# Kernel tuning notes

Hardware: AMD Instinct MI355X
Metric: run time of the kernel (lower is better)

The kernel has to match this reference:

```python
import jax, jax.numpy as jnp
import numpy as np

NEG_INF = -1e20  # the repo defines INF = 1e20
TOPK = 10


def setup_inputs() -> dict:
    key = jax.random.key(0)
    k1, k2 = jax.random.split(key)
    B, N, D, H = 8, 2048, 512, 512
    context = jax.random.normal(k1, (B, N, D), dtype=jnp.float32)
    ctx_mask = jnp.ones((B, N), dtype=jnp.int32)  # all positions valid
    W = jax.random.normal(k2, (H, D), dtype=jnp.float32) * 0.02  # linear_sim weight
    return {"context": context, "W": W, "ctx_mask": ctx_mask}


def reference(context, W, ctx_mask):
    # context_fc = relu(linear_sim(context))        : [B, N, H]
    ctx_fc = jax.nn.relu(jnp.einsum('bnd,hd->bnh', context, W))
    # attention = context_fc @ context_fc^T         : [B, N, N]
    att = jnp.einsum('bnh,bmh->bnm', ctx_fc, ctx_fc)
    # masked_fill where ctx_mask == 0 (both row and column)
    m = ctx_mask.astype(bool)
    att = jnp.where(m[:, None, :], att, NEG_INF)
    att = jnp.where(m[:, :, None], att, NEG_INF)
    # build_knn_neighbourhood: keep top-k per row, everything else -INF
    k = min(TOPK, att.shape[-1])
    knn_val, knn_ind = jax.lax.top_k(att, k)  # [B, N, k]
    B, N, _ = att.shape
    bi = jnp.arange(B)[:, None, None]
    ri = jnp.arange(N)[None, :, None]
    adj = jnp.full(att.shape, NEG_INF, dtype=att.dtype).at[bi, ri, knn_ind].set(knn_val)
    return adj
```

## Files before the change

kernel.cpp:

```cpp
#include <hip/hip_runtime.h>
#include <hip/hip_bf16.h>

#define NEG_INF -1e20f

typedef __bf16 bf16x8 __attribute__((ext_vector_type(8)));
typedef float  f32x4  __attribute__((ext_vector_type(4)));

__device__ inline unsigned short f2bf(float x) {
    unsigned u = __float_as_uint(x);
    unsigned r = u + 0x7fffu + ((u >> 16) & 1u);
    return (unsigned short)(r >> 16);
}
__device__ inline float bf2f(unsigned short h) {
    return __uint_as_float((unsigned)h << 16);
}
__device__ inline unsigned fkey(float f) {
    unsigned u = __float_as_uint(f);
    return (u & 0x80000000u) ? ~u : (u | 0x80000000u);
}
__device__ inline float unfkey(unsigned k) {
    unsigned fu = (k & 0x80000000u) ? (k ^ 0x80000000u) : ~k;
    return __uint_as_float(fu);
}

__global__ __launch_bounds__(256) void split3_all(
        const float* __restrict__ ctx, const float* __restrict__ W,
        unsigned short* __restrict__ C1, unsigned short* __restrict__ C2,
        unsigned short* __restrict__ C3, unsigned short* __restrict__ W1,
        unsigned short* __restrict__ W2, unsigned short* __restrict__ W3) {
    const int b = blockIdx.x;
    const int t = threadIdx.x;
    const float* src;
    unsigned short *p1, *p2, *p3;
    int base;
    if (b < 2048) { src = ctx; p1 = C1; p2 = C2; p3 = C3; base = b * 1024; }
    else          { src = W;   p1 = W1; p2 = W2; p3 = W3; base = (b - 2048) * 1024; }
#pragma unroll
    for (int it = 0; it < 4; ++it) {
        int i = base + it * 256 + t;
        float4 v = ((const float4*)src)[i];
        ushort4 a, bb, c;
        float r;
        a.x = f2bf(v.x); r = v.x - bf2f(a.x); bb.x = f2bf(r); c.x = f2bf(r - bf2f(bb.x));
        a.y = f2bf(v.y); r = v.y - bf2f(a.y); bb.y = f2bf(r); c.y = f2bf(r - bf2f(bb.y));
        a.z = f2bf(v.z); r = v.z - bf2f(a.z); bb.z = f2bf(r); c.z = f2bf(r - bf2f(bb.z));
        a.w = f2bf(v.w); r = v.w - bf2f(a.w); bb.w = f2bf(r); c.w = f2bf(r - bf2f(bb.w));
        ((ushort4*)p1)[i] = a;
        ((ushort4*)p2)[i] = bb;
        ((ushort4*)p3)[i] = c;
    }
}

__global__ __launch_bounds__(256, 2) void fc_mfma6(
        const unsigned short* __restrict__ A1, const unsigned short* __restrict__ A2,
        const unsigned short* __restrict__ A3, const unsigned short* __restrict__ B1,
        const unsigned short* __restrict__ B2, const unsigned short* __restrict__ B3,
        unsigned short* __restrict__ Fhi, unsigned short* __restrict__ Flo) {
    __shared__ char lds[49152];

    const int t     = threadIdx.x;
    const int mBase = blockIdx.x * 128;
    const int hBase = blockIdx.y * 128;
    const int w = t >> 6, lane = t & 63;
    const int q = lane >> 4, ln = lane & 15;
    const int wn = (w >> 1) * 64;
    const int wm = (w & 1) * 64;

    f32x4 acc[4][4] = {};

    for (int kt = 0; kt < 512; kt += 32) {
#pragma unroll
        for (int p = 0; p < 3; ++p) {
            const unsigned short* pl = (p == 0) ? A1 : (p == 1) ? A2 : A3;
#pragma unroll
            for (int rr = 0; rr < 2; ++rr) {
                int chunk = rr * 256 + t;
                int row   = chunk >> 2;
                int c     = (chunk & 3) ^ ((row >> 1) & 3);
                const unsigned short* g = pl + ((size_t)(mBase + row) * 512 + kt + c * 8);
                char* l = lds + p * 8192 + chunk * 16;
                __builtin_amdgcn_global_load_lds(
                    (const __attribute__((address_space(1))) void*)g,
                    (__attribute__((address_space(3))) void*)l, 16, 0, 0);
            }
        }
#pragma unroll
        for (int p = 0; p < 3; ++p) {
            const unsigned short* pl = (p == 0) ? B1 : (p == 1) ? B2 : B3;
#pragma unroll
            for (int rr = 0; rr < 2; ++rr) {
                int chunk = rr * 256 + t;
                int row   = chunk >> 2;
                int c     = (chunk & 3) ^ ((row >> 1) & 3);
                const unsigned short* g = pl + ((size_t)(hBase + row) * 512 + kt + c * 8);
                char* l = lds + 24576 + p * 8192 + chunk * 16;
                __builtin_amdgcn_global_load_lds(
                    (const __attribute__((address_space(1))) void*)g,
                    (__attribute__((address_space(3))) void*)l, 16, 0, 0);
            }
        }
        __syncthreads();

        bf16x8 a1[4], a2[4], a3[4], b1[4], b2[4], b3[4];
#pragma unroll
        for (int i = 0; i < 4; ++i) {
            int mA = wn + i * 16 + ln;
            int oA = (mA * 4 + (q ^ ((mA >> 1) & 3))) * 16;
            a1[i] = *(const bf16x8*)(lds +     0 + oA);
            a2[i] = *(const bf16x8*)(lds +  8192 + oA);
            a3[i] = *(const bf16x8*)(lds + 16384 + oA);
            int mB = wm + i * 16 + ln;
            int oB = (mB * 4 + (q ^ ((mB >> 1) & 3))) * 16;
            b1[i] = *(const bf16x8*)(lds + 24576 + oB);
            b2[i] = *(const bf16x8*)(lds + 32768 + oB);
            b3[i] = *(const bf16x8*)(lds + 40960 + oB);
        }
#pragma unroll
        for (int i = 0; i < 4; ++i)
#pragma unroll
            for (int j = 0; j < 4; ++j) {
                acc[i][j] = __builtin_amdgcn_mfma_f32_16x16x32_bf16(a1[i], b1[j], acc[i][j], 0, 0, 0);
                acc[i][j] = __builtin_amdgcn_mfma_f32_16x16x32_bf16(a1[i], b2[j], acc[i][j], 0, 0, 0);
                acc[i][j] = __builtin_amdgcn_mfma_f32_16x16x32_bf16(a2[i], b1[j], acc[i][j], 0, 0, 0);
                acc[i][j] = __builtin_amdgcn_mfma_f32_16x16x32_bf16(a2[i], b2[j], acc[i][j], 0, 0, 0);
                acc[i][j] = __builtin_amdgcn_mfma_f32_16x16x32_bf16(a1[i], b3[j], acc[i][j], 0, 0, 0);
                acc[i][j] = __builtin_amdgcn_mfma_f32_16x16x32_bf16(a3[i], b1[j], acc[i][j], 0, 0, 0);
            }
        __syncthreads();
    }

    unsigned* tb = (unsigned*)(lds + w * 4352);
    const int rg = lane >> 4;
    const int c4 = lane & 15;
#pragma unroll
    for (int i = 0; i < 4; ++i) {
#pragma unroll
        for (int j = 0; j < 4; ++j)
#pragma unroll
            for (int r = 0; r < 4; ++r) {
                float v = fmaxf(acc[i][j][r], 0.f);
                unsigned short hi = f2bf(v);
                unsigned short lo = f2bf(v - bf2f(hi));
                tb[(q * 4 + r) * 68 + j * 16 + ln] =
                    (unsigned)hi | ((unsigned)lo << 16);
            }
#pragma unroll
        for (int it = 0; it < 4; ++it) {
            int row = it * 4 + rg;
            uint4 pk = *(const uint4*)&tb[row * 68 + c4 * 4];
            ushort4 h, l;
            h.x = (unsigned short)pk.x; l.x = (unsigned short)(pk.x >> 16);
            h.y = (unsigned short)pk.y; l.y = (unsigned short)(pk.y >> 16);
            h.z = (unsigned short)pk.z; l.z = (unsigned short)(pk.z >> 16);
            h.w = (unsigned short)pk.w; l.w = (unsigned short)(pk.w >> 16);
            size_t off = (size_t)(mBase + wn + i * 16 + row) * 512 + hBase + wm + c4 * 4;
            *(ushort4*)(Fhi + off) = h;
            *(ushort4*)(Flo + off) = l;
        }
    }
}

__global__ __launch_bounds__(256, 3) void att_sym_cand(
        const unsigned short* __restrict__ Fhi, const unsigned short* __restrict__ Flo,
        const int* __restrict__ mask, float* __restrict__ out,
        float* __restrict__ cv2) {
    __shared__ char lds[32768];

    const int t = threadIdx.x;
    const int b = blockIdx.x & 7;
    int p = blockIdx.x >> 3, ti = 0;
    while (p >= 16 - ti) { p -= 16 - ti; ++ti; }
    const int tj = ti + p;
    const int nBase = ti * 128;
    const int mBase = tj * 128;
    const int w    = t >> 6, lane = t & 63;
    const int q    = lane >> 4, ln = lane & 15;
    const int wn   = (w >> 1) * 64;
    const int wm   = (w & 1) * 64;
    const size_t rowB = (size_t)b * 2048;

    f32x4 acc[4][4] = {};

    for (int kt = 0; kt < 512; kt += 32) {
#pragma unroll
        for (int pp = 0; pp < 4; ++pp) {
            const unsigned short* plane = (pp & 1) ? Flo : Fhi;
            int rbase = (pp < 2) ? nBase : mBase;
#pragma unroll
            for (int r = 0; r < 2; ++r) {
                int chunk = r * 256 + t;
                int row   = chunk >> 2;
                int c     = (chunk & 3) ^ ((row >> 1) & 3);
                const unsigned short* g =
                    plane + ((rowB + rbase + row) * 512 + kt + c * 8);
                char* l = lds + pp * 8192 + chunk * 16;
                __builtin_amdgcn_global_load_lds(
                    (const __attribute__((address_space(1))) void*)g,
                    (__attribute__((address_space(3))) void*)l, 16, 0, 0);
            }
        }
        __syncthreads();

        bf16x8 ah[4], al[4], bh[4], bl[4];
#pragma unroll
        for (int i = 0; i < 4; ++i) {
            int mA = wn + i * 16 + ln;
            int oA = (mA * 4 + (q ^ ((mA >> 1) & 3))) * 16;
            ah[i] = *(const bf16x8*)(lds +     0 + oA);
            al[i] = *(const bf16x8*)(lds +  8192 + oA);
            int mB = wm + i * 16 + ln;
            int oB = (mB * 4 + (q ^ ((mB >> 1) & 3))) * 16;
            bh[i] = *(const bf16x8*)(lds + 16384 + oB);
            bl[i] = *(const bf16x8*)(lds + 24576 + oB);
        }
#pragma unroll
        for (int i = 0; i < 4; ++i)
#pragma unroll
            for (int j = 0; j < 4; ++j) {
                acc[i][j] = __builtin_amdgcn_mfma_f32_16x16x32_bf16(ah[i], bh[j], acc[i][j], 0, 0, 0);
                acc[i][j] = __builtin_amdgcn_mfma_f32_16x16x32_bf16(ah[i], bl[j], acc[i][j], 0, 0, 0);
                acc[i][j] = __builtin_amdgcn_mfma_f32_16x16x32_bf16(al[i], bh[j], acc[i][j], 0, 0, 0);
            }
        __syncthreads();
    }

    const int* mb = mask + b * 2048;
    float* outB = out + (size_t)b * 2048 * 2048;
    int cmj[4];
#pragma unroll
    for (int j = 0; j < 4; ++j) cmj[j] = mb[mBase + wm + j * 16 + ln];
    int rmAll[4][4];
#pragma unroll
    for (int i = 0; i < 4; ++i)
#pragma unroll
        for (int r = 0; r < 4; ++r) rmAll[i][r] = mb[nBase + wn + i * 16 + q * 4 + r];

    float* tb = (float*)(lds + w * 4352);
    const int rg = lane >> 4;
    const int c4 = lane & 15;
    const bool mirror = (ti != tj);
#pragma unroll
    for (int i = 0; i < 4; ++i) {
        int n0 = nBase + wn + i * 16;
#pragma unroll
        for (int r = 0; r < 4; ++r) {
            float m4 = NEG_INF;
#pragma unroll
            for (int j = 0; j < 4; ++j) {
                float v = ((rmAll[i][r] != 0) & (cmj[j] != 0)) ? acc[i][j][r] : NEG_INF;
                m4 = fmaxf(m4, v);
            }
            m4 = fmaxf(m4, __shfl_xor(m4, 1, 64));
            m4 = fmaxf(m4, __shfl_xor(m4, 2, 64));
            m4 = fmaxf(m4, __shfl_xor(m4, 4, 64));
            m4 = fmaxf(m4, __shfl_xor(m4, 8, 64));
            if (ln == 0)
                cv2[(rowB + n0 + q * 4 + r) * 32 + tj * 2 + (w & 1)] = m4;
        }
#pragma unroll
        for (int j = 0; j < 4; ++j)
#pragma unroll
            for (int r = 0; r < 4; ++r) {
                float v = ((rmAll[i][r] != 0) & (cmj[j] != 0)) ? acc[i][j][r] : NEG_INF;
                tb[(q * 4 + r) * 68 + j * 16 + ln] = v;
            }
#pragma unroll
        for (int it = 0; it < 4; ++it) {
            int row = it * 4 + rg;
            float4 vv = *(const float4*)&tb[row * 68 + c4 * 4];
            *(float4*)(outB + (size_t)(n0 + row) * 2048 + mBase + wm + c4 * 4) = vv;
        }
        if (mirror) {
#pragma unroll
            for (int ps = 0; ps < 4; ++ps) {
                float4 mv;
                mv.x = tb[(ps * 4 + 0) * 68 + lane];
                mv.y = tb[(ps * 4 + 1) * 68 + lane];
                mv.z = tb[(ps * 4 + 2) * 68 + lane];
                mv.w = tb[(ps * 4 + 3) * 68 + lane];
                *(float4*)(outB + (size_t)(mBase + wm + lane) * 2048 + n0 + ps * 4) = mv;
            }
        }
    }
    if (mirror) {
#pragma unroll
        for (int j = 0; j < 4; ++j) {
            float m16 = NEG_INF;
#pragma unroll
            for (int i2 = 0; i2 < 4; ++i2)
#pragma unroll
                for (int r = 0; r < 4; ++r) {
                    float v = ((rmAll[i2][r] != 0) & (cmj[j] != 0)) ? acc[i2][j][r] : NEG_INF;
                    m16 = fmaxf(m16, v);
                }
            m16 = fmaxf(m16, __shfl_xor(m16, 16, 64));
            m16 = fmaxf(m16, __shfl_xor(m16, 32, 64));
            if (q == 0)
                cv2[(rowB + mBase + wm + j * 16 + ln) * 32 + ti * 2 + (w >> 1)] = m16;
        }
    }
}

__global__ __launch_bounds__(256) void topk_filter(
        const float* __restrict__ cv2, float* __restrict__ att) {
    __shared__ float2 surv[4][64];
    __shared__ float2 win[4][10];

    const int t = threadIdx.x, w = t >> 6, lane = t & 63;
    const size_t R = (size_t)blockIdx.x * 4 + w;
    float* row = att + R * 2048;

    float cnd = (lane < 32) ? cv2[R * 32 + lane] : NEG_INF;
    int rk = 0;
#pragma unroll
    for (int j = 0; j < 32; ++j) {
        float vj = __shfl(cnd, j, 64);
        rk += ((vj > cnd) || (vj == cnd && j < lane)) ? 1 : 0;
    }
    unsigned long long bl = __ballot((lane < 32) && (rk == 9));
    float L = __shfl(cnd, __ffsll(bl) - 1, 64);
    unsigned long long hsel = __ballot((lane < 32) && (cnd >= L));
    const int nsel = (int)__popcll(hsel);

    const bool ok = (nsel <= 16);
    float v[16]; int hcol[16]; bool hv[16];
    if (ok) {
        unsigned long long m = hsel;
#pragma unroll
        for (int k = 0; k < 16; ++k) {
            hv[k] = (m != 0);
            int h = hv[k] ? (__ffsll(m) - 1) : 0;
            m &= (m - 1);
            hcol[k] = h * 64 + lane;
            v[k] = row[h * 64 + lane];
        }
    }

    int nsurv = 0;
    if (ok) {
        const unsigned long long lmask = (1ull << lane) - 1;
#pragma unroll
        for (int k = 0; k < 16; ++k) {
            bool pr = hv[k] && (v[k] >= L);
            unsigned long long pb = __ballot(pr);
            if (pr) {
                int idx = nsurv + (int)__popcll(pb & lmask);
                if (idx < 64) surv[w][idx] = make_float2(v[k], __int_as_float(hcol[k]));
            }
            nsurv += (int)__popcll(pb);
        }
    }

    if (ok && nsurv <= 64) {
        float sv = NEG_INF; int sc = 0x7fffffff;
        if (lane < nsurv) {
            float2 s2 = surv[w][lane];
            sv = s2.x; sc = __float_as_int(s2.y);
        }
        int r2 = 0;
        for (int j = 0; j < nsurv; ++j) {
            float2 sj = surv[w][j];
            int cj = __float_as_int(sj.y);
            r2 += ((sj.x > sv) || (sj.x == sv && cj < sc)) ? 1 : 0;
        }
        if ((lane < nsurv) && (r2 < 10))
            win[w][r2] = make_float2(sv, __int_as_float(sc));
    } else {
        unsigned key[32];
#pragma unroll
        for (int s = 0; s < 8; ++s) {
            float4 vv = *(const float4*)(row + lane * 32 + s * 4);
            key[s * 4 + 0] = fkey(vv.x);
            key[s * 4 + 1] = fkey(vv.y);
            key[s * 4 + 2] = fkey(vv.z);
            key[s * 4 + 3] = fkey(vv.w);
        }
        unsigned h1 = key[0]; int i1 = 0;
#pragma unroll
        for (int j = 1; j < 32; ++j)
            if (key[j] > h1) { h1 = key[j]; i1 = j; }
        unsigned h2 = 0; int i2 = 0;
#pragma unroll
        for (int j = 0; j < 32; ++j) {
            bool okb = (j != i1) && (key[j] > h2);
            h2 = okb ? key[j] : h2;
            i2 = okb ? j : i2;
        }
        bool h2valid = true;
        unsigned taken = 0;
        for (int r = 0; r < 10; ++r) {
            unsigned M = h1;
#pragma unroll
            for (int off = 1; off < 64; off <<= 1) {
                unsigned o = __shfl_xor(M, off, 64);
                M = (o > M) ? o : M;
            }
            unsigned long long ball = __ballot(h1 == M);
            int srcb = __ffsll(ball) - 1;
            int wloc = __shfl(i1, srcb, 64);
            if (lane == r) win[w][r] = make_float2(unfkey(M), __int_as_float(srcb * 32 + wloc));
            if (lane == srcb) {
                taken |= 1u << i1;
                if (h2valid) { h1 = h2; i1 = i2; h2valid = false; }
                else {
                    unsigned bh = 0; int bi = 0;
#pragma unroll
                    for (int j = 0; j < 32; ++j) {
                        bool okb = (((taken >> j) & 1u) == 0u) && (key[j] > bh);
                        bh = okb ? key[j] : bh;
                        bi = okb ? j : bi;
                    }
                    h1 = bh; i1 = bi;
                }
            }
        }
    }

    float wv[10]; int wc[10];
#pragma unroll
    for (int k = 0; k < 10; ++k) {
        float2 wk = win[w][k];
        wv[k] = wk.x; wc[k] = __float_as_int(wk.y);
    }

#pragma unroll
    for (int s = 0; s < 8; ++s) {
        float4 f4 = make_float4(NEG_INF, NEG_INF, NEG_INF, NEG_INF);
        int cb = s * 256 + lane * 4;
#pragma unroll
        for (int k = 0; k < 10; ++k) {
            if ((wc[k] >> 8) == s) {
                f4.x = (wc[k] == cb + 0) ? wv[k] : f4.x;
                f4.y = (wc[k] == cb + 1) ? wv[k] : f4.y;
                f4.z = (wc[k] == cb + 2) ? wv[k] : f4.z;
                f4.w = (wc[k] == cb + 3) ? wv[k] : f4.w;
            }
        }
        ((float4*)row)[s * 64 + lane] = f4;
    }
}

extern "C" void kernel_launch(void* const* d_in, const int* in_sizes, int n_in,
                              void* d_out, int out_size, void* d_ws, size_t ws_size,
                              hipStream_t stream) {
    const float* ctx  = (const float*)d_in[0];
    const float* W    = (const float*)d_in[1];
    const int*   mask = (const int*)d_in[2];
    float* out = (float*)d_out;

    const size_t CN = (size_t)16384 * 512;
    const size_t WN = (size_t)512 * 512;
    unsigned short* C1 = (unsigned short*)d_out;
    unsigned short* C2 = C1 + CN;
    unsigned short* C3 = C2 + CN;
    unsigned short* W1 = C3 + CN;
    unsigned short* W2 = W1 + WN;
    unsigned short* W3 = W2 + WN;

    float* cv2 = (float*)d_ws;
    unsigned short* Fhi = (unsigned short*)(cv2 + (size_t)16384 * 32);
    unsigned short* Flo = Fhi + CN;

    dim3 blk(256);
    split3_all<<<dim3(2112), blk, 0, stream>>>(ctx, W, C1, C2, C3, W1, W2, W3);
    fc_mfma6<<<dim3(128, 4), blk, 0, stream>>>(C1, C2, C3, W1, W2, W3, Fhi, Flo);
    att_sym_cand<<<dim3(1088), blk, 0, stream>>>(Fhi, Flo, mask, out, cv2);
    topk_filter<<<dim3(4096), blk, 0, stream>>>(cv2, out);
}
```

Before: 295.2 us.

## Double-buffer fc GEMM with 512-thread 256x128 tiles and async LDS prefetch

Rewrites the context-projection GEMM kernel to use 512 threads covering a 256x128 output tile. Global-to-LDS loads are double-buffered in dynamic shared memory (about 144KB), and the next K-slice is prefetched while MFMAs run on the current one. The block-wide barriers become explicit vmcnt waits plus s_barrier, and s_setprio is raised around the MFMA section. The aim is to hide load latency and cut synchronisation stalls, at the cost of one block per CU and a large LDS footprint. The epilogue still appears to index LDS per wave, and it is unclear whether the existing epilogue handles the 8 waves and 256-row tile correctly.

```diff
diff --git a/kernel.cpp b/kernel.cpp
--- a/kernel.cpp
+++ b/kernel.cpp
@@ -51,70 +51,79 @@
     }
 }
 
-__global__ __launch_bounds__(256, 2) void fc_mfma6(
+__global__ __launch_bounds__(512, 1) void fc_8ph(
         const unsigned short* __restrict__ A1, const unsigned short* __restrict__ A2,
         const unsigned short* __restrict__ A3, const unsigned short* __restrict__ B1,
         const unsigned short* __restrict__ B2, const unsigned short* __restrict__ B3,
         unsigned short* __restrict__ Fhi, unsigned short* __restrict__ Flo) {
-    __shared__ char lds[49152];
+    extern __shared__ char lds[];
 
     const int t     = threadIdx.x;
-    const int mBase = blockIdx.x * 128;
+    const int mBase = blockIdx.x * 256;
     const int hBase = blockIdx.y * 128;
     const int w = t >> 6, lane = t & 63;
     const int q = lane >> 4, ln = lane & 15;
     const int wn = (w >> 1) * 64;
     const int wm = (w & 1) * 64;
 
-    f32x4 acc[4][4] = {};
-
-    for (int kt = 0; kt < 512; kt += 32) {
-#pragma unroll
-        for (int p = 0; p < 3; ++p) {
-            const unsigned short* pl = (p == 0) ? A1 : (p == 1) ? A2 : A3;
+    const unsigned short* Ap[3] = {A1, A2, A3};
+    const unsigned short* Bp[3] = {B1, B2, B3};
+
+    auto stage = [&](int kt, char* buf) {
+#pragma unroll
+        for (int p = 0; p < 3; ++p)
 #pragma unroll
             for (int rr = 0; rr < 2; ++rr) {
-                int chunk = rr * 256 + t;
-                int row   = chunk >> 2;
-                int c     = (chunk & 3) ^ ((row >> 1) & 3);
-                const unsigned short* g = pl + ((size_t)(mBase + row) * 512 + kt + c * 8);
-                char* l = lds + p * 8192 + chunk * 16;
+                int ch  = rr * 512 + t;
+                int row = ch >> 2;
+                int c   = (ch & 3) ^ ((row >> 1) & 3);
+                const unsigned short* g = Ap[p] + ((size_t)(mBase + row) * 512 + kt + c * 8);
                 __builtin_amdgcn_global_load_lds(
                     (const __attribute__((address_space(1))) void*)g,
-                    (__attribute__((address_space(3))) void*)l, 16, 0, 0);
-            }
-        }
+                    (__attribute__((address_space(3))) void*)(buf + p * 16384 + ch * 16),
+                    16, 0, 0);
+            }
 #pragma unroll
         for (int p = 0; p < 3; ++p) {
-            const unsigned short* pl = (p == 0) ? B1 : (p == 1) ? B2 : B3;
-#pragma unroll
-            for (int rr = 0; rr < 2; ++rr) {
-                int chunk = rr * 256 + t;
-                int row   = chunk >> 2;
-                int c     = (chunk & 3) ^ ((row >> 1) & 3);
-                const unsigned short* g = pl + ((size_t)(hBase + row) * 512 + kt + c * 8);
-                char* l = lds + 24576 + p * 8192 + chunk * 16;
-                __builtin_amdgcn_global_load_lds(
-                    (const __attribute__((address_space(1))) void*)g,
-                    (__attribute__((address_space(3))) void*)l, 16, 0, 0);
-            }
-        }
-        __syncthreads();
+            int ch  = t;
+            int row = ch >> 2;
+            int c   = (ch & 3) ^ ((row >> 1) & 3);
+            const unsigned short* g = Bp[p] + ((size_t)(hBase + row) * 512 + kt + c * 8);
+            __builtin_amdgcn_global_load_lds(
+                (const __attribute__((address_space(1))) void*)g,
+                (__attribute__((address_space(3))) void*)(buf + 49152 + p * 8192 + ch * 16),
+                16, 0, 0);
+        }
+    };
+
+    f32x4 acc[4][4] = {};
+
+    stage(0,  lds);
+    stage(32, lds + 73728);
+
+    for (int tt = 0; tt < 16; ++tt) {
+        char* buf = lds + (tt & 1) * 73728;
+        if (tt < 15) asm volatile("s_waitcnt vmcnt(9)" ::: "memory");
+        else         asm volatile("s_waitcnt vmcnt(0)" ::: "memory");
+        __builtin_amdgcn_sched_barrier(0);
+        __builtin_amdgcn_s_barrier();
+        __builtin_amdgcn_sched_barrier(0);
 
         bf16x8 a1[4], a2[4], a3[4], b1[4], b2[4], b3[4];
 #pragma unroll
         for (int i = 0; i < 4; ++i) {
             int mA = wn + i * 16 + ln;
             int oA = (mA * 4 + (q ^ ((mA >> 1) & 3))) * 16;
-            a1[i] = *(const bf16x8*)(lds +     0 + oA);
-            a2[i] = *(const bf16x8*)(lds +  8192 + oA);
-            a3[i] = *(const bf16x8*)(lds + 16384 + oA);
+            a1[i] = *(const bf16x8*)(buf +     0 + oA);
+            a2[i] = *(const bf16x8*)(buf + 16384 + oA);
+            a3[i] = *(const bf16x8*)(buf + 32768 + oA);
             int mB = wm + i * 16 + ln;
             int oB = (mB * 4 + (q ^ ((mB >> 1) & 3))) * 16;
-            b1[i] = *(const bf16x8*)(lds + 24576 + oB);
-            b2[i] = *(const bf16x8*)(lds + 32768 + oB);
-            b3[i] = *(const bf16x8*)(lds + 40960 + oB);
-        }
+            b1[i] = *(const bf16x8*)(buf + 49152 + oB);
+            b2[i] = *(const bf16x8*)(buf + 57344 + oB);
+            b3[i] = *(const bf16x8*)(buf + 65536 + oB);
+        }
+        __builtin_amdgcn_s_setprio(1);
 #pragma unroll
         for (int i = 0; i < 4; ++i)
 #pragma unroll
@@ -126,7 +135,10 @@
                 acc[i][j] = __builtin_amdgcn_mfma_f32_16x16x32_bf16(a1[i], b3[j], acc[i][j], 0, 0, 0);
                 acc[i][j] = __builtin_amdgcn_mfma_f32_16x16x32_bf16(a3[i], b1[j], acc[i][j], 0, 0, 0);
             }
-        __syncthreads();
+        __builtin_amdgcn_s_setprio(0);
+        __builtin_amdgcn_sched_barrier(0);
+        __builtin_amdgcn_s_barrier();
+        if (tt < 14) stage((tt + 2) * 32, buf);
     }
 
     unsigned* tb = (unsigned*)(lds + w * 4352);
@@ -461,9 +473,17 @@
     unsigned short* Fhi = (unsigned short*)(cv2 + (size_t)16384 * 32);
     unsigned short* Flo = Fhi + CN;
 
+    static bool s_attr = false;
+    if (!s_attr) {
+        (void)hipFuncSetAttribute((const void*)fc_8ph,
+                                  hipFuncAttributeMaxDynamicSharedMemorySize,
+                                  2 * 73728);
+        s_attr = true;
+    }
+
     dim3 blk(256);
     split3_all<<<dim3(2112), blk, 0, stream>>>(ctx, W, C1, C2, C3, W1, W2, W3);
-    fc_mfma6<<<dim3(128, 4), blk, 0, stream>>>(C1, C2, C3, W1, W2, W3, Fhi, Flo);
+    fc_8ph<<<dim3(64, 4), dim3(512), 2 * 73728, stream>>>(C1, C2, C3, W1, W2, W3, Fhi, Flo);
     att_sym_cand<<<dim3(1088), blk, 0, stream>>>(Fhi, Flo, mask, out, cv2);
     topk_filter<<<dim3(4096), blk, 0, stream>>>(cv2, out);
 }
```

New measurement: 299.0 us. Within noise of the previous version (+1.3%).

## Double-buffer LDS tiles with async global_load_lds prefetch in symmetric attention GEMM

Applied to the files above, without the earlier changes.

Splits the K-loop into two 32 KB LDS buffers and prefetches tile k+2 while MFMAs consume tile k, using explicit vmcnt waits and raw s_barrier instead of __syncthreads. The goal is to hide global-load latency behind the bf16 split-precision MFMA work. It also raises wave priority around the MFMA block. The cost is that LDS grows to 64 KB, so launch bounds drop from 3 to 2 blocks per CU, which lowers occupancy.

```diff
diff --git a/kernel.cpp b/kernel.cpp
--- a/kernel.cpp
+++ b/kernel.cpp
@@ -160,11 +160,11 @@
     }
 }
 
-__global__ __launch_bounds__(256, 3) void att_sym_cand(
+__global__ __launch_bounds__(256, 2) void att_sym_cand(
         const unsigned short* __restrict__ Fhi, const unsigned short* __restrict__ Flo,
         const int* __restrict__ mask, float* __restrict__ out,
         float* __restrict__ cv2) {
-    __shared__ char lds[32768];
+    __shared__ char lds[65536];
 
     const int t = threadIdx.x;
     const int b = blockIdx.x & 7;
@@ -179,9 +179,7 @@
     const int wm   = (w & 1) * 64;
     const size_t rowB = (size_t)b * 2048;
 
-    f32x4 acc[4][4] = {};
-
-    for (int kt = 0; kt < 512; kt += 32) {
+    auto stage = [&](int kt, char* buf) {
 #pragma unroll
         for (int pp = 0; pp < 4; ++pp) {
             const unsigned short* plane = (pp & 1) ? Flo : Fhi;
@@ -193,26 +191,40 @@
                 int c     = (chunk & 3) ^ ((row >> 1) & 3);
                 const unsigned short* g =
                     plane + ((rowB + rbase + row) * 512 + kt + c * 8);
-                char* l = lds + pp * 8192 + chunk * 16;
                 __builtin_amdgcn_global_load_lds(
                     (const __attribute__((address_space(1))) void*)g,
-                    (__attribute__((address_space(3))) void*)l, 16, 0, 0);
-            }
-        }
-        __syncthreads();
+                    (__attribute__((address_space(3))) void*)(buf + pp * 8192 + chunk * 16),
+                    16, 0, 0);
+            }
+        }
+    };
+
+    f32x4 acc[4][4] = {};
+
+    stage(0,  lds);
+    stage(32, lds + 32768);
+
+    for (int tt = 0; tt < 16; ++tt) {
+        char* buf = lds + (tt & 1) * 32768;
+        if (tt < 15) asm volatile("s_waitcnt vmcnt(8)" ::: "memory");
+        else         asm volatile("s_waitcnt vmcnt(0)" ::: "memory");
+        __builtin_amdgcn_sched_barrier(0);
+        __builtin_amdgcn_s_barrier();
+        __builtin_amdgcn_sched_barrier(0);
 
         bf16x8 ah[4], al[4], bh[4], bl[4];
 #pragma unroll
         for (int i = 0; i < 4; ++i) {
             int mA = wn + i * 16 + ln;
             int oA = (mA * 4 + (q ^ ((mA >> 1) & 3))) * 16;
-            ah[i] = *(const bf16x8*)(lds +     0 + oA);
-            al[i] = *(const bf16x8*)(lds +  8192 + oA);
+            ah[i] = *(const bf16x8*)(buf +     0 + oA);
+            al[i] = *(const bf16x8*)(buf +  8192 + oA);
             int mB = wm + i * 16 + ln;
             int oB = (mB * 4 + (q ^ ((mB >> 1) & 3))) * 16;
-            bh[i] = *(const bf16x8*)(lds + 16384 + oB);
-            bl[i] = *(const bf16x8*)(lds + 24576 + oB);
-        }
+            bh[i] = *(const bf16x8*)(buf + 16384 + oB);
+            bl[i] = *(const bf16x8*)(buf + 24576 + oB);
+        }
+        __builtin_amdgcn_s_setprio(1);
 #pragma unroll
         for (int i = 0; i < 4; ++i)
 #pragma unroll
@@ -221,7 +233,10 @@
                 acc[i][j] = __builtin_amdgcn_mfma_f32_16x16x32_bf16(ah[i], bl[j], acc[i][j], 0, 0, 0);
                 acc[i][j] = __builtin_amdgcn_mfma_f32_16x16x32_bf16(al[i], bh[j], acc[i][j], 0, 0, 0);
             }
-        __syncthreads();
+        __builtin_amdgcn_s_setprio(0);
+        __builtin_amdgcn_sched_barrier(0);
+        __builtin_amdgcn_s_barrier();
+        if (tt < 14) stage((tt + 2) * 32, buf);
     }
 
     const int* mb = mask + b * 2048;
```

Result: slower. 302.4 us (+2.4%).
